# Optimization experiments

Hardware: AMD Instinct MI355X
Metric: run time of the kernel (lower is better)

Reference implementation:

```python
import jax, jax.numpy as jnp
import numpy as np
import math

NUM_SPHERICAL = 7
NUM_RADIAL = 6
CUTOFF = 5.0
ENV_EXP = 5
N_EDGES = 200000
N_QUADS = 400000

# ---- numpy-side precomputation of spherical Bessel zeros / normalizers ----

def _sph_jn_np(n, x):
    # spherical Bessel j_n via upward recurrence (stable for x > n here)
    j0 = np.sin(x) / x
    if n == 0:
        return j0
    j1 = np.sin(x) / x**2 - np.cos(x) / x
    jm1, jc = j0, j1
    for l in range(1, n):
        jm1, jc = jc, (2 * l + 1) / x * jc - jm1
    return jc

def _jn_zeros(n, k):
    # roots of j_l for l=0..n-1, using interlacing + bisection (as in DimeNet Jn_zeros)
    zerosj = np.zeros((n, k))
    zerosj[0] = np.arange(1, k + 1) * np.pi
    points = np.arange(1, k + n) * np.pi
    for order in range(1, n):
        nroots = k + n - 1 - order
        racines = np.zeros(nroots)
        for j in range(nroots):
            a, b = points[j], points[j + 1]
            fa = _sph_jn_np(order, a)
            for _ in range(80):
                m = 0.5 * (a + b)
                fm = _sph_jn_np(order, m)
                if fa * fm <= 0:
                    b = m
                else:
                    a, fa = m, fm
            racines[j] = 0.5 * (a + b)
        points = racines
        zerosj[order] = racines[:k]
    return zerosj

_Z = _jn_zeros(NUM_SPHERICAL, NUM_RADIAL)  # [S, R] roots z_{l,j}
_BNORM = np.zeros((NUM_SPHERICAL, NUM_RADIAL))
for _l in range(NUM_SPHERICAL):
    for _j in range(NUM_RADIAL):
        _BNORM[_l, _j] = 1.0 / np.sqrt(0.5 * _sph_jn_np(_l + 1, _Z[_l, _j]) ** 2)

# repeat-by-degree index: l repeated (2l+1) times -> length S^2
_L_INDEX = np.repeat(np.arange(NUM_SPHERICAL), 2 * np.arange(NUM_SPHERICAL) + 1)

# ---- jax helpers ----

def _sph_jn(n, x):
    j0 = jnp.sin(x) / x
    if n == 0:
        return j0
    j1 = jnp.sin(x) / x**2 - jnp.cos(x) / x
    jm1, jc = j0, j1
    for l in range(1, n):
        jm1, jc = jc, (2.0 * l + 1.0) / x * jc - jm1
    return jc

def _real_sph_harm(theta, phi, S):
    # real spherical harmonics Y_lm(theta, phi) for l < S, all m (zero_m_only=False)
    # column order per l: m=0, m=1..l (cos branch), m=-l..-1 (sin branch)
    ct, st = jnp.cos(theta), jnp.sin(theta)
    P = [[None] * (l + 1) for l in range(S)]
    P[0][0] = jnp.ones_like(ct)
    for m in range(S):
        if m > 0:
            P[m][m] = (1.0 - 2.0 * m) * st * P[m - 1][m - 1]
        if m + 1 < S:
            P[m + 1][m] = (2.0 * m + 1.0) * ct * P[m][m]
        for l in range(m + 2, S):
            P[l][m] = ((2.0 * l - 1.0) * ct * P[l - 1][m] - (l + m - 1.0) * P[l - 2][m]) / (l - m)
    cols = []
    for l in range(S):
        def K(m):
            return math.sqrt((2 * l + 1) / (4 * math.pi) * math.factorial(l - m) / math.factorial(l + m))
        cols.append(K(0) * P[l][0])
        for m in range(1, l + 1):
            cols.append(math.sqrt(2.0) * K(m) * jnp.cos(m * phi) * P[l][m])
        for m in range(l, 0, -1):  # negative m = -l..-1
            cols.append(math.sqrt(2.0) * K(m) * jnp.sin(m * phi) * P[l][m])
    return jnp.stack(cols, axis=1)  # [Q, S^2]


def setup_inputs() -> dict:
    key = jax.random.key(0)
    k1, k2, k3, k4, k5 = jax.random.split(key, 5)
    D_ca = 0.5 + jax.random.uniform(k1, (N_EDGES,), jnp.float32) * (CUTOFF - 0.5)
    Alpha_cab = jax.random.uniform(k2, (N_QUADS,), jnp.float32) * np.pi
    Theta_cabd = jax.random.uniform(k3, (N_QUADS,), jnp.float32) * (2.0 * np.pi)
    id4_reduce_ca = jax.random.randint(k4, (N_QUADS,), 0, N_EDGES)
    Kidx = jax.random.randint(k5, (N_QUADS,), 0, 16)
    return {"D_ca": D_ca, "Alpha_cab": Alpha_cab, "Theta_cabd": Theta_cabd,
            "id4_reduce_ca": id4_reduce_ca, "Kidx": Kidx}


def reference(D_ca, Alpha_cab, Theta_cabd, id4_reduce_ca, Kidx):
    S, R = NUM_SPHERICAL, NUM_RADIAL
    inv_cutoff = 1.0 / CUTOFF
    d = D_ca * inv_cutoff  # [E]

    # envelope u(d) = (1/d + a d^(p-1) + b d^p + c d^(p+1)) * 1[d<1]
    p = ENV_EXP + 1
    a = -(p + 1) * (p + 2) / 2.0
    b = float(p * (p + 2))
    c = -p * (p + 1) / 2.0
    u_d = jnp.where(d < 1.0, 1.0 / d + a * d ** (p - 1) + b * d ** p + c * d ** (p + 1), 0.0)

    # radial Bessel basis rbf[e, l, j] = norm_{l,j} * j_l(z_{l,j} * d_e) * cutoff^{-3/2}
    norm_const = inv_cutoff ** 1.5
    rbf_l = []
    for l in range(S):
        xl = d[:, None] * jnp.asarray(_Z[l], d.dtype)  # [E, R]
        rbf_l.append(jnp.asarray(_BNORM[l], d.dtype) * _sph_jn(l, xl))
    rbf = jnp.stack(rbf_l, axis=1) * norm_const  # [E, S, R]
    rbf_env = u_d[:, None, None] * rbf           # [E, S, R]

    # repeat degree l block (2l+1) times -> [E, S^2, R], flatten -> [E, S^2*R]
    rbf_env = rbf_env[:, _L_INDEX, :].reshape(-1, S * S * R)
    rbf_env = rbf_env[id4_reduce_ca]             # gather -> [Q, S^2*R]

    sph = _real_sph_harm(Alpha_cab, Theta_cabd, S)  # [Q, S^2]
    sph = jnp.repeat(sph, R, axis=1)                # [Q, S^2*R]
    return rbf_env * sph
```

## Files before the change

kernel.cpp:

```cpp
#include <hip/hip_runtime.h>
#include <cmath>

#ifndef M_PI
#define M_PI 3.14159265358979323846
#endif

#define NS 7
#define NR 6
#define NSPH 49
#define NRB 42
#define NOUT 294
#define QPB 64
#define NTHREADS 512
#define RBF_PAD 44
#define SPH_PAD 50

typedef float vfloat4 __attribute__((ext_vector_type(4)));

struct Consts {
  float zb[NS][NR];
  float bn[NS][NR];
  float kc[NS][NS];
};

static double sph_jn_d(int n, double x) {
  double j0 = sin(x) / x;
  if (n == 0) return j0;
  double j1 = sin(x) / (x * x) - cos(x) / x;
  double jm1 = j0, jc = j1;
  for (int l = 1; l < n; ++l) {
    double nx = (2.0 * l + 1.0) / x * jc - jm1;
    jm1 = jc; jc = nx;
  }
  return jc;
}

static Consts make_consts() {
  Consts C;
  double zeros[NS][NR];
  double points[NS + NR];
  for (int j = 0; j < NR; ++j) zeros[0][j] = (j + 1) * M_PI;
  for (int i = 0; i < NS + NR - 1; ++i) points[i] = (i + 1) * M_PI;
  for (int order = 1; order < NS; ++order) {
    int nroots = NR + NS - 1 - order;
    double racines[NS + NR];
    for (int j = 0; j < nroots; ++j) {
      double a = points[j], b = points[j + 1];
      double fa = sph_jn_d(order, a);
      for (int it = 0; it < 80; ++it) {
        double m = 0.5 * (a + b);
        double fm = sph_jn_d(order, m);
        if (fa * fm <= 0.0) b = m;
        else { a = m; fa = fm; }
      }
      racines[j] = 0.5 * (a + b);
    }
    for (int j = 0; j < nroots; ++j) points[j] = racines[j];
    for (int j = 0; j < NR; ++j) zeros[order][j] = racines[j];
  }
  const double norm_const = pow(1.0 / 5.0, 1.5);
  for (int l = 0; l < NS; ++l)
    for (int j = 0; j < NR; ++j) {
      C.zb[l][j] = (float)zeros[l][j];
      double jn1 = sph_jn_d(l + 1, zeros[l][j]);
      C.bn[l][j] = (float)(1.0 / sqrt(0.5 * jn1 * jn1) * norm_const);
    }
  double fact[16]; fact[0] = 1.0;
  for (int i = 1; i < 16; ++i) fact[i] = fact[i - 1] * i;
  for (int l = 0; l < NS; ++l)
    for (int m = 0; m < NS; ++m) {
      if (m > l) { C.kc[l][m] = 0.f; continue; }
      double K = sqrt((2.0 * l + 1.0) / (4.0 * M_PI) * fact[l - m] / fact[l + m]);
      C.kc[l][m] = (float)((m == 0) ? K : sqrt(2.0) * K);
    }
  return C;
}

__global__ __launch_bounds__(NTHREADS, 4)
void tensor_basis_kernel(const float* __restrict__ D,
                         const float* __restrict__ Alpha,
                         const float* __restrict__ Theta,
                         const int* __restrict__ id4,
                         float* __restrict__ out,
                         int nq, Consts C) {
  __shared__ float s_d[QPB], s_u[QPB];
  __shared__ float s_rbf[QPB][RBF_PAD];
  __shared__ float s_sph[QPB][SPH_PAD];
  __shared__ unsigned short s_tab[NOUT];
  __shared__ float s_zb[NRB], s_bn[NRB];

  const int tid = threadIdx.x;
  const int q0 = blockIdx.x * QPB;

  if (tid < QPB) {
    int q = q0 + tid;
    float alpha = 0.f, theta = 0.f;
    if (q < nq) { alpha = Alpha[q]; theta = Theta[q]; }
    float st, ct; sincosf(alpha, &st, &ct);
    float sp, cp; sincosf(theta, &sp, &cp);
    float P[NS][NS];
    P[0][0] = 1.f;
#pragma unroll
    for (int m = 0; m < NS; ++m) {
      if (m > 0) P[m][m] = (1.f - 2.f * (float)m) * st * P[m - 1][m - 1];
      if (m + 1 < NS) P[m + 1][m] = (2.f * (float)m + 1.f) * ct * P[m][m];
#pragma unroll
      for (int l = m + 2; l < NS; ++l)
        P[l][m] = ((2.f * (float)l - 1.f) * ct * P[l - 1][m] -
                   (float)(l + m - 1) * P[l - 2][m]) / (float)(l - m);
    }
    float cm[NS], sm[NS];
    cm[0] = 1.f; sm[0] = 0.f;
    cm[1] = cp;  sm[1] = sp;
#pragma unroll
    for (int m = 2; m < NS; ++m) {
      cm[m] = 2.f * cp * cm[m - 1] - cm[m - 2];
      sm[m] = 2.f * cp * sm[m - 1] - sm[m - 2];
    }
    int idx = 0;
#pragma unroll
    for (int l = 0; l < NS; ++l) {
      s_sph[tid][idx++] = C.kc[l][0] * P[l][0];
#pragma unroll
      for (int m = 1; m <= l; ++m)
        s_sph[tid][idx++] = C.kc[l][m] * cm[m] * P[l][m];
#pragma unroll
      for (int m = l; m >= 1; --m)
        s_sph[tid][idx++] = C.kc[l][m] * sm[m] * P[l][m];
    }
  } else if (tid < 2 * QPB) {
    int lq = tid - QPB;
    int q = q0 + lq;
    float d = 0.5f, u = 0.f;
    if (q < nq) {
      int e = id4[q];
      d = D[e] * 0.2f;
      float d2 = d * d, d4 = d2 * d2, d5 = d4 * d;
      u = (d < 1.f) ? (1.f / d + d5 * (-28.f + d * (48.f - 21.f * d))) : 0.f;
    }
    s_d[lq] = d;
    s_u[lq] = u;
  } else {
    int t = tid - 2 * QPB;
    if (t < NOUT) {
      int s = t / NR;
      int j = t - NR * s;
      int l = (int)sqrtf((float)s + 0.5f);
      s_tab[t] = (unsigned short)((s << 8) | (l * NR + j));
    } else if (t < NOUT + NRB) {
      int u2 = t - NOUT;
      s_zb[u2] = ((const float*)C.zb)[u2];
      s_bn[u2] = ((const float*)C.bn)[u2];
    }
  }
  __syncthreads();

  if (tid >= QPB) {
    int t = tid - QPB;
#pragma unroll
    for (int k = 0; k < 6; ++k) {
      int task = t + k * 448;
      int ql = task / NRB;
      int idx = task - ql * NRB;
      int l = idx / NR;
      float d = s_d[ql];
      float x = d * s_zb[idx];
      float sx, cx; sincosf(x, &sx, &cx);
      float invx = 1.f / x;
      float jl = sx * invx;
      if (l > 0) {
        float jm1 = jl;
        float jc = sx * invx * invx - cx * invx;
        for (int ll = 1; ll < l; ++ll) {
          float nx = (2.f * (float)ll + 1.f) * invx * jc - jm1;
          jm1 = jc; jc = nx;
        }
        jl = jc;
      }
      s_rbf[ql][idx] = s_u[ql] * s_bn[idx] * jl;
    }
  }
  __syncthreads();

  const int ebase = q0 * NOUT;
  const int tot = nq * NOUT;
  auto do4 = [&](int f) {
    int e = 4 * f;
    int ql = e / NOUT;
    int i0 = e - ql * NOUT;
    float v[4];
#pragma unroll
    for (int c = 0; c < 4; ++c) {
      int ii = i0 + c, qq = ql;
      if (ii >= NOUT) { ii -= NOUT; ++qq; }
      unsigned t2 = s_tab[ii];
      v[c] = s_rbf[qq][t2 & 0xFFu] * s_sph[qq][t2 >> 8];
    }
    int g = ebase + e;
    if (g + 3 < tot) {
      vfloat4 pv; pv.x = v[0]; pv.y = v[1]; pv.z = v[2]; pv.w = v[3];
      __builtin_nontemporal_store(pv, reinterpret_cast<vfloat4*>(out + g));
    } else {
#pragma unroll
      for (int c = 0; c < 4; ++c)
        if (g + c < tot) out[g + c] = v[c];
    }
  };
#pragma unroll 3
  for (int it = 0; it < 9; ++it) do4(tid + it * NTHREADS);
  {
    int f = tid + 9 * NTHREADS;
    if (f < (QPB * NOUT) / 4) do4(f);
  }
}

extern "C" void kernel_launch(void* const* d_in, const int* in_sizes, int n_in,
                              void* d_out, int out_size, void* d_ws, size_t ws_size,
                              hipStream_t stream) {
  (void)n_in; (void)out_size; (void)d_ws; (void)ws_size;
  static const Consts C = make_consts();
  const float* D     = (const float*)d_in[0];
  const float* Alpha = (const float*)d_in[1];
  const float* Theta = (const float*)d_in[2];
  const int*   id4   = (const int*)d_in[3];
  float* out = (float*)d_out;
  const int nq = in_sizes[1];
  const int blocks = (nq + QPB - 1) / QPB;
  hipLaunchKernelGGL(tensor_basis_kernel, dim3(blocks), dim3(NTHREADS), 0, stream,
                     D, Alpha, Theta, id4, out, nq, C);
}
```

Measured before the change: 474.1 us.

## Shrink blocks to one wavefront with 32 quads and rebalance per-thread work

Cuts the block from 512 threads and 64 quads to 64 threads and 32 quads. Within that single wavefront, half the lanes compute spherical harmonics and half compute the envelope; all lanes then share the Bessel evaluations and the output writes. This changes the work split so each block is one wave with a short critical path and more blocks in flight. In exchange, each thread does far more serial loop iterations and sph computation occupies only half the lanes, which diverges within the wave.

After: 522.3 us. +10.2%, slower.

```diff
diff --git a/kernel.cpp b/kernel.cpp
--- a/kernel.cpp
+++ b/kernel.cpp
@@ -7,11 +7,10 @@
 
 #define NS 7
 #define NR 6
-#define NSPH 49
 #define NRB 42
 #define NOUT 294
-#define QPB 64
-#define NTHREADS 512
+#define QPB 32
+#define NTHREADS 64
 #define RBF_PAD 44
 #define SPH_PAD 50
 
@@ -76,7 +75,7 @@
   return C;
 }
 
-__global__ __launch_bounds__(NTHREADS, 4)
+__global__ __launch_bounds__(NTHREADS, 6)
 void tensor_basis_kernel(const float* __restrict__ D,
                          const float* __restrict__ Alpha,
                          const float* __restrict__ Theta,
@@ -92,43 +91,17 @@
   const int tid = threadIdx.x;
   const int q0 = blockIdx.x * QPB;
 
-  if (tid < QPB) {
-    int q = q0 + tid;
-    float alpha = 0.f, theta = 0.f;
-    if (q < nq) { alpha = Alpha[q]; theta = Theta[q]; }
-    float st, ct; sincosf(alpha, &st, &ct);
-    float sp, cp; sincosf(theta, &sp, &cp);
-    float P[NS][NS];
-    P[0][0] = 1.f;
-#pragma unroll
-    for (int m = 0; m < NS; ++m) {
-      if (m > 0) P[m][m] = (1.f - 2.f * (float)m) * st * P[m - 1][m - 1];
-      if (m + 1 < NS) P[m + 1][m] = (2.f * (float)m + 1.f) * ct * P[m][m];
-#pragma unroll
-      for (int l = m + 2; l < NS; ++l)
-        P[l][m] = ((2.f * (float)l - 1.f) * ct * P[l - 1][m] -
-                   (float)(l + m - 1) * P[l - 2][m]) / (float)(l - m);
-    }
-    float cm[NS], sm[NS];
-    cm[0] = 1.f; sm[0] = 0.f;
-    cm[1] = cp;  sm[1] = sp;
-#pragma unroll
-    for (int m = 2; m < NS; ++m) {
-      cm[m] = 2.f * cp * cm[m - 1] - cm[m - 2];
-      sm[m] = 2.f * cp * sm[m - 1] - sm[m - 2];
-    }
-    int idx = 0;
-#pragma unroll
-    for (int l = 0; l < NS; ++l) {
-      s_sph[tid][idx++] = C.kc[l][0] * P[l][0];
-#pragma unroll
-      for (int m = 1; m <= l; ++m)
-        s_sph[tid][idx++] = C.kc[l][m] * cm[m] * P[l][m];
-#pragma unroll
-      for (int m = l; m >= 1; --m)
-        s_sph[tid][idx++] = C.kc[l][m] * sm[m] * P[l][m];
-    }
-  } else if (tid < 2 * QPB) {
+  for (int t = tid; t < NOUT; t += NTHREADS) {
+    int s = t / NR, j = t - NR * s;
+    int l = (int)sqrtf((float)s + 0.5f);
+    s_tab[t] = (unsigned short)((s << 8) | (l * NR + j));
+  }
+  if (tid < NRB) {
+    s_zb[tid] = ((const float*)C.zb)[tid];
+    s_bn[tid] = ((const float*)C.bn)[tid];
+  }
+
+  if (tid >= QPB) {
     int lq = tid - QPB;
     int q = q0 + lq;
     float d = 0.5f, u = 0.f;
@@ -141,44 +114,65 @@
     s_d[lq] = d;
     s_u[lq] = u;
   } else {
-    int t = tid - 2 * QPB;
-    if (t < NOUT) {
-      int s = t / NR;
-      int j = t - NR * s;
-      int l = (int)sqrtf((float)s + 0.5f);
-      s_tab[t] = (unsigned short)((s << 8) | (l * NR + j));
-    } else if (t < NOUT + NRB) {
-      int u2 = t - NOUT;
-      s_zb[u2] = ((const float*)C.zb)[u2];
-      s_bn[u2] = ((const float*)C.bn)[u2];
+    int q = q0 + tid;
+    float alpha = 0.f, theta = 0.f;
+    if (q < nq) { alpha = Alpha[q]; theta = Theta[q]; }
+    float st, ct; sincosf(alpha, &st, &ct);
+    float sp, cp; sincosf(theta, &sp, &cp);
+    float P[NS][NS];
+    P[0][0] = 1.f;
+#pragma unroll
+    for (int m = 0; m < NS; ++m) {
+      if (m > 0) P[m][m] = (1.f - 2.f * (float)m) * st * P[m - 1][m - 1];
+      if (m + 1 < NS) P[m + 1][m] = (2.f * (float)m + 1.f) * ct * P[m][m];
+#pragma unroll
+      for (int l = m + 2; l < NS; ++l)
+        P[l][m] = ((2.f * (float)l - 1.f) * ct * P[l - 1][m] -
+                   (float)(l + m - 1) * P[l - 2][m]) / (float)(l - m);
+    }
+    float cm[NS], sm[NS];
+    cm[0] = 1.f; sm[0] = 0.f;
+    cm[1] = cp;  sm[1] = sp;
+#pragma unroll
+    for (int m = 2; m < NS; ++m) {
+      cm[m] = 2.f * cp * cm[m - 1] - cm[m - 2];
+      sm[m] = 2.f * cp * sm[m - 1] - sm[m - 2];
+    }
+    int idx = 0;
+#pragma unroll
+    for (int l = 0; l < NS; ++l) {
+      s_sph[tid][idx++] = C.kc[l][0] * P[l][0];
+#pragma unroll
+      for (int m = 1; m <= l; ++m)
+        s_sph[tid][idx++] = C.kc[l][m] * cm[m] * P[l][m];
+#pragma unroll
+      for (int m = l; m >= 1; --m)
+        s_sph[tid][idx++] = C.kc[l][m] * sm[m] * P[l][m];
     }
   }
   __syncthreads();
 
-  if (tid >= QPB) {
-    int t = tid - QPB;
-#pragma unroll
-    for (int k = 0; k < 6; ++k) {
-      int task = t + k * 448;
-      int ql = task / NRB;
-      int idx = task - ql * NRB;
-      int l = idx / NR;
-      float d = s_d[ql];
-      float x = d * s_zb[idx];
-      float sx, cx; sincosf(x, &sx, &cx);
-      float invx = 1.f / x;
-      float jl = sx * invx;
-      if (l > 0) {
-        float jm1 = jl;
-        float jc = sx * invx * invx - cx * invx;
-        for (int ll = 1; ll < l; ++ll) {
-          float nx = (2.f * (float)ll + 1.f) * invx * jc - jm1;
-          jm1 = jc; jc = nx;
-        }
-        jl = jc;
+#pragma unroll 3
+  for (int k = 0; k < 21; ++k) {
+    int task = k * NTHREADS + tid;
+    unsigned ql  = (unsigned)task / (unsigned)NRB;
+    unsigned idx = (unsigned)task - ql * NRB;
+    unsigned l   = idx / (unsigned)NR;
+    float d = s_d[ql];
+    float x = d * s_zb[idx];
+    float sx, cx; sincosf(x, &sx, &cx);
+    float invx = 1.f / x;
+    float jl = sx * invx;
+    if (l > 0) {
+      float jm1 = jl;
+      float jc = sx * invx * invx - cx * invx;
+      for (unsigned ll = 1; ll < l; ++ll) {
+        float nx = (2.f * (float)ll + 1.f) * invx * jc - jm1;
+        jm1 = jc; jc = nx;
       }
-      s_rbf[ql][idx] = s_u[ql] * s_bn[idx] * jl;
-    }
+      jl = jc;
+    }
+    s_rbf[ql][idx] = s_u[ql] * s_bn[idx] * jl;
   }
   __syncthreads();
 
@@ -206,12 +200,9 @@
         if (g + c < tot) out[g + c] = v[c];
     }
   };
-#pragma unroll 3
-  for (int it = 0; it < 9; ++it) do4(tid + it * NTHREADS);
-  {
-    int f = tid + 9 * NTHREADS;
-    if (f < (QPB * NOUT) / 4) do4(f);
-  }
+#pragma unroll 4
+  for (int it = 0; it < 36; ++it) do4(it * NTHREADS + tid);
+  if (tid < 48) do4(36 * NTHREADS + tid);
 }
 
 extern "C" void kernel_launch(void* const* d_in, const int* in_sizes, int n_in,
```
